# Kernel tuning notes

Measured on AMD Instinct MI355X. Metric: run time of the kernel, lower is better.

Reference implementation:

```python
import jax, jax.numpy as jnp
import numpy as np

N = 8192        # batch_size (number of nodes)
E = 262144      # number of edges
VD = 256        # vertex_dim
ED = 256        # edge_dim
HD = 512        # hid_dim
DAMPING = 0.45
EPS = 1e-5      # BatchNorm1d default eps


def setup_inputs() -> dict:
    key = jax.random.key(0)
    ks = jax.random.split(key, 8)
    def lin_w(k, out_d, in_d):
        # kaiming-uniform-ish scale, fp32
        lim = 1.0 / np.sqrt(in_d)
        return jax.random.uniform(k, (out_d, in_d), jnp.float32, -lim, lim)
    return {
        "x": jax.random.normal(ks[0], (N, VD), jnp.float32),
        "edge_weight": jax.random.normal(ks[1], (E, ED), jnp.float32),
        "edge_index": jax.random.randint(ks[2], (2, E), 0, N),
        "W0": lin_w(ks[3], HD, VD), "b0": jnp.zeros((HD,), jnp.float32),
        "Ww0": lin_w(ks[4], HD, ED), "bw0": jnp.zeros((HD,), jnp.float32),
        "W1": lin_w(ks[5], VD, HD), "b1": jnp.zeros((VD,), jnp.float32),
        "Ww1": lin_w(ks[6], ED, HD), "bw1": jnp.zeros((ED,), jnp.float32),
        "gamma": jnp.ones((HD,), jnp.float32),
        "beta": jnp.zeros((HD,), jnp.float32),
    }


def reference(x, edge_weight, edge_index, W0, b0, Ww0, bw0, W1, b1, Ww1, bw1, gamma, beta):
    out = x @ W0.T + b0                       # [N, HD]
    w = edge_weight @ Ww0.T + bw0             # [E, HD]
    src = edge_index[0]                       # [E]
    # The per-node python loop in the original is an exact segment reduction:
    # out[i] += damping * sum of w over edges with src==i (pre-update w),
    # then w[e] += damping * scalar_sum(out_new[src[e]])  (t.sum over hid dim).
    out = out + DAMPING * jax.ops.segment_sum(w, src, num_segments=N)
    node_scalar = jnp.sum(out, axis=1)        # [N] scalar per node
    w = w + DAMPING * node_scalar[src][:, None]
    # cauchy selector: cosine similarity minus identity, row-softmax mix
    nrm = jnp.sqrt(jnp.sum(out * out, axis=1, keepdims=True))   # [N,1]
    sim = (out @ out.T) / (nrm @ nrm.T) - jnp.eye(N, dtype=out.dtype)
    out = jax.nn.softmax(sim, axis=1) @ out   # [N, HD]
    # BatchNorm1d in training mode (batch stats, biased variance)
    mean = jnp.mean(w, axis=0)
    var = jnp.mean((w - mean) ** 2, axis=0)
    w = (w - mean) * jax.lax.rsqrt(var + EPS) * gamma + beta
    return out @ W1.T + b1, w @ Ww1.T + bw1
```

## Files before the change

kernel.cpp:

```cpp
#include <hip/hip_runtime.h>

typedef unsigned short u16;
typedef __attribute__((ext_vector_type(8))) short bh8;
typedef __attribute__((ext_vector_type(4))) short bh4;
typedef __attribute__((ext_vector_type(4))) float f4v;

#define NN 8192
#define EE 262144
#define VDIM 256
#define EDIM 256
#define HDIM 512
#define DAMP 0.45f

__device__ __forceinline__ float b2f(u16 u){ unsigned int x = ((unsigned int)u)<<16; return __builtin_bit_cast(float, x); }
__device__ __forceinline__ u16 f2b(float f){ unsigned int x = __builtin_bit_cast(unsigned int, f); x = (x + 0x7fffu + ((x>>16)&1u)) >> 16; return (u16)x; }

__device__ __forceinline__ void gload16(const void* g, void* l){
  __builtin_amdgcn_global_load_lds((const __attribute__((address_space(1))) void*)g,
                                   (__attribute__((address_space(3))) void*)l, 16, 0, 0);
}

__global__ __launch_bounds__(256) void k_hist(const int* __restrict__ src, int* __restrict__ deg){
  int e = blockIdx.x*256 + threadIdx.x;
  if (e < EE) atomicAdd(&deg[src[e]], 1);
}

__global__ __launch_bounds__(1024) void k_scan(const int* __restrict__ deg, int* __restrict__ ofs, int* __restrict__ cur){
  __shared__ int lds[1024];
  int t = threadIdx.x;
  int v[8], pre[8]; int s = 0;
  #pragma unroll
  for (int j=0;j<8;++j){ v[j] = deg[t*8+j]; }
  #pragma unroll
  for (int j=0;j<8;++j){ pre[j] = s; s += v[j]; }
  lds[t] = s; __syncthreads();
  int run = s;
  for (int off=1; off<1024; off<<=1){
    int x = (t>=off) ? lds[t-off] : 0;
    __syncthreads();
    lds[t] += x;
    __syncthreads();
  }
  int excl = lds[t] - run;
  #pragma unroll
  for (int j=0;j<8;++j){ int o = excl + pre[j]; ofs[t*8+j] = o; cur[t*8+j] = o; }
  if (t == 1023) ofs[NN] = excl + run;
}

__global__ __launch_bounds__(256) void k_permute(const int* __restrict__ src, int* __restrict__ cur,
                                                 int* __restrict__ pos, int* __restrict__ elist){
  int e = blockIdx.x*256 + threadIdx.x;
  if (e < EE){ int p = atomicAdd(&cur[src[e]], 1); pos[e] = p; elist[p] = e; }
}

__global__ __launch_bounds__(256) void k_cvtW(const float* __restrict__ in, u16* __restrict__ out, int n8){
  int i = blockIdx.x*256 + threadIdx.x;
  if (i < n8){
    const f4v* p = (const f4v*)(in + (size_t)i*8);
    f4v f0 = p[0], f1 = p[1];
    bh8 v;
    #pragma unroll
    for (int j=0;j<4;++j){ v[j]=(short)f2b(f0[j]); v[j+4]=(short)f2b(f1[j]); }
    ((bh8*)out)[i] = v;
  }
}

template<int A_BF16, int B_BF16, int EPI>
__global__ __launch_bounds__(256)
void k_gemm(const void* __restrict__ Aptr, const void* __restrict__ Bptr,
            int M, int N, int K, const float* __restrict__ bias,
            void* __restrict__ Cptr,
            const float* __restrict__ invnA, float* __restrict__ lsum)
{
  __shared__ u16 As[2][128*32];
  __shared__ u16 Bs[2][128*32];
  __shared__ float lrow[128];
  const int t = threadIdx.x;
  const int m0 = blockIdx.y*128, n0 = blockIdx.x*128;
  const int wid = t>>6, lane = t&63, l15 = lane&15, grp = lane>>4;
  const int wm = (wid>>1)*64, wn = (wid&1)*64;
  const int srow = t>>1, shalf = t&1;
  const int rlane = lane>>2, clane = lane&3;

  if (EPI == 3 && t < 128) lrow[t] = 0.f;

  f4v acc[4][4];
  #pragma unroll
  for (int i=0;i<4;++i)
    #pragma unroll
    for (int j=0;j<4;++j) acc[i][j] = (f4v)0.0f;

  auto stage = [&](int buf, int kt){
    if (A_BF16){
      const u16* g0 = (const u16*)Aptr + (size_t)(m0 + wid*32 + rlane)*K + kt + clane*8;
      gload16(g0,                 &As[buf][wid*1024]);
      gload16(g0 + (size_t)16*K,  &As[buf][wid*1024 + 512]);
    } else {
      u16* dst = &As[buf][srow*32 + shalf*16];
      const float* ap = (const float*)Aptr + (size_t)(m0+srow)*K + kt + shalf*16;
      const f4v* ap4 = (const f4v*)ap;
      f4v f0 = ap4[0], f1 = ap4[1], f2 = ap4[2], f3 = ap4[3];
      bh8 v0, v1;
      #pragma unroll
      for (int j=0;j<4;++j){ v0[j]=(short)f2b(f0[j]); v0[j+4]=(short)f2b(f1[j]); v1[j]=(short)f2b(f2[j]); v1[j+4]=(short)f2b(f3[j]); }
      ((bh8*)dst)[0] = v0; ((bh8*)dst)[1] = v1;
    }
    if (B_BF16){
      const u16* g0 = (const u16*)Bptr + (size_t)(n0 + wid*32 + rlane)*K + kt + clane*8;
      gload16(g0,                 &Bs[buf][wid*1024]);
      gload16(g0 + (size_t)16*K,  &Bs[buf][wid*1024 + 512]);
    } else {
      u16* dst = &Bs[buf][srow*32 + shalf*16];
      const float* bp = (const float*)Bptr + (size_t)(n0+srow)*K + kt + shalf*16;
      const f4v* bp4 = (const f4v*)bp;
      f4v f0 = bp4[0], f1 = bp4[1], f2 = bp4[2], f3 = bp4[3];
      bh8 v0, v1;
      #pragma unroll
      for (int j=0;j<4;++j){ v0[j]=(short)f2b(f0[j]); v0[j+4]=(short)f2b(f1[j]); v1[j]=(short)f2b(f2[j]); v1[j+4]=(short)f2b(f3[j]); }
      ((bh8*)dst)[0] = v0; ((bh8*)dst)[1] = v1;
    }
  };

  stage(0, 0);
  __syncthreads();
  int cur = 0;
  for (int kt=0; kt<K; kt+=32){
    if (kt + 32 < K) stage(cur^1, kt+32);
    bh8 af[4], bfv[4];
    #pragma unroll
    for (int f=0; f<4; ++f) af[f]  = *(const bh8*)&As[cur][(wm + f*16 + l15)*32 + grp*8];
    #pragma unroll
    for (int f=0; f<4; ++f) bfv[f] = *(const bh8*)&Bs[cur][(wn + f*16 + l15)*32 + grp*8];
    #pragma unroll
    for (int fi=0; fi<4; ++fi)
      #pragma unroll
      for (int fj=0; fj<4; ++fj)
        acc[fi][fj] = __builtin_amdgcn_mfma_f32_16x16x32_bf16(af[fi], bfv[fj], acc[fi][fj], 0, 0, 0);
    __syncthreads();
    cur ^= 1;
  }

  if (EPI == 3){
    float ic[4];
    #pragma unroll
    for (int fj=0; fj<4; ++fj) ic[fj] = invnA[n0 + wn + fj*16 + l15];
    #pragma unroll
    for (int fi=0; fi<4; ++fi){
      #pragma unroll
      for (int r=0;r<4;++r){
        int rowg = m0 + wm + fi*16 + grp*4 + r;
        float iq = invnA[rowg];
        float rs = 0.f;
        #pragma unroll
        for (int fj=0; fj<4; ++fj){
          int c = n0 + wn + fj*16 + l15;
          float s = acc[fi][fj][r]*iq*ic[fj];
          float p = (rowg == c) ? 1.0f : __expf(s);
          ((u16*)Cptr)[(size_t)rowg*N + c] = f2b(p);
          rs += p;
        }
        rs += __shfl_xor(rs,1); rs += __shfl_xor(rs,2); rs += __shfl_xor(rs,4); rs += __shfl_xor(rs,8);
        if (l15 == 0) atomicAdd(&lrow[wm + fi*16 + grp*4 + r], rs);
      }
    }
    __syncthreads();
    if (t < 128) lsum[(size_t)blockIdx.x*NN + m0 + t] = lrow[t];
    return;
  }

  float ilv[4][4];
  if (EPI == 4){
    #pragma unroll
    for (int fi=0; fi<4; ++fi)
      #pragma unroll
      for (int r=0;r<4;++r)
        ilv[fi][r] = 1.0f / lsum[m0 + wm + fi*16 + grp*4 + r];
  }
  #pragma unroll
  for (int fj=0; fj<4; ++fj){
    int c = n0 + wn + fj*16 + l15;
    float bv = (EPI == 0 && bias) ? bias[c] : 0.f;
    #pragma unroll
    for (int fi=0; fi<4; ++fi){
      #pragma unroll
      for (int r=0;r<4;++r){
        size_t rowg = (size_t)(m0 + wm + fi*16 + grp*4 + r);
        float v = acc[fi][fj][r];
        if (EPI == 0)      ((float*)Cptr)[rowg*N + c] = v + bv;
        else               ((u16*)Cptr)[rowg*N + c]  = f2b(v * ilv[fi][r]);
      }
    }
  }
}

__global__ __launch_bounds__(256)
void k_lred(const float* __restrict__ lpart, float* __restrict__ lsum){
  int i = blockIdx.x*256 + threadIdx.x;
  float s = 0.f;
  #pragma unroll 8
  for (int b = 0; b < 64; ++b) s += lpart[(size_t)b*NN + i];
  lsum[i] = s;
}

template<int A_BF16, int BN, int EPI>
__global__ __launch_bounds__(512, 4)
void k_gemmw3(const void* __restrict__ Aptr, const u16* __restrict__ Bptr,
              int K, const float* __restrict__ bias, void* __restrict__ Cptr,
              const int* __restrict__ mapArr, const int* __restrict__ srcIdx,
              const float* __restrict__ nsArr, const float* __restrict__ rowterm,
              const float* __restrict__ constterm)
{
  constexpr int CG = BN/64;
  constexpr int MF = (CG==8)?4:2;
  __shared__ u16 As[64*32];
  __shared__ u16 Bs[BN*32];
  const int t = threadIdx.x;
  const int tile = ((int)blockIdx.x & 7)*((int)gridDim.x>>3) + ((int)blockIdx.x>>3);
  const int m0 = tile*64;
  const int wid = t>>6, lane = t&63, l15 = lane&15, grp = lane>>4;
  const int wn = (wid & (CG-1))*64;
  const int wm = (wid / CG)*32;

  f4v acc[MF][4];
  #pragma unroll
  for (int i=0;i<MF;++i)
    #pragma unroll
    for (int j=0;j<4;++j) acc[i][j] = (f4v)0.0f;

  if (A_BF16){
    if (wid < 4){
      const u16* g0 = (const u16*)Aptr + (size_t)(m0 + wid*16 + (lane>>2))*K + (lane&3)*8;
      gload16(g0, &As[wid*512]);
    }
  } else {
    const float* ap = (const float*)Aptr + (size_t)(m0 + (t>>3))*K + (t&7)*4;
    f4v f0 = *(const f4v*)ap;
    bh4 v;
    #pragma unroll
    for (int j=0;j<4;++j) v[j]=(short)f2b(f0[j]);
    *(bh4*)&As[(t>>3)*32 + (t&7)*4] = v;
  }
  #pragma unroll
  for (int j=0;j<BN/128;++j){
    const u16* g0 = Bptr + (size_t)(j*128 + wid*16 + (lane>>2))*K + (lane&3)*8;
    gload16(g0, &Bs[wid*512 + j*4096]);
  }
  __syncthreads();

  for (int kt=0; kt<K; kt+=32){
    const bool more = (kt+32 < K);
    f4v pf; bh8 pb;
    if (more){
      if (A_BF16){
        if (t < 256)
          pb = *(const bh8*)((const u16*)Aptr + (size_t)(m0 + (t>>2))*K + kt+32 + (t&3)*8);
      } else {
        pf = *(const f4v*)((const float*)Aptr + (size_t)(m0 + (t>>3))*K + kt+32 + (t&7)*4);
      }
    }
    bh8 af[MF], bfv[4];
    #pragma unroll
    for (int f=0; f<MF; ++f) af[f]  = *(const bh8*)&As[(wm + f*16 + l15)*32 + grp*8];
    #pragma unroll
    for (int f=0; f<4; ++f)  bfv[f] = *(const bh8*)&Bs[(wn + f*16 + l15)*32 + grp*8];
    #pragma unroll
    for (int fi=0; fi<MF; ++fi)
      #pragma unroll
      for (int fj=0; fj<4; ++fj)
        acc[fi][fj] = __builtin_amdgcn_mfma_f32_16x16x32_bf16(af[fi], bfv[fj], acc[fi][fj], 0, 0, 0);
    __syncthreads();
    if (more){
      if (A_BF16){
        if (t < 256) *(bh8*)&As[(t>>2)*32 + (t&3)*8] = pb;
      } else {
        bh4 v;
        #pragma unroll
        for (int j=0;j<4;++j) v[j]=(short)f2b(pf[j]);
        *(bh4*)&As[(t>>3)*32 + (t&7)*4] = v;
      }
      #pragma unroll
      for (int j=0;j<BN/128;++j){
        const u16* g0 = Bptr + (size_t)(j*128 + wid*16 + (lane>>2))*K + kt+32 + (lane&3)*8;
        gload16(g0, &Bs[wid*512 + j*4096]);
      }
    }
    __syncthreads();
  }

  #pragma unroll
  for (int fi=0; fi<MF; ++fi){
    #pragma unroll
    for (int r=0;r<4;++r){
      int slot = m0 + wm + fi*16 + grp*4 + r;
      int mp = mapArr[slot];
      float cv = (EPI == 2) ? DAMP * nsArr[srcIdx[mp]] : 0.f;
      #pragma unroll
      for (int fj=0; fj<4; ++fj){
        int c = wn + fj*16 + l15;
        if (EPI == 5) ((u16*)Cptr)[(size_t)mp*BN + c]  = f2b(acc[fi][fj][r] + bias[c]);
        else          ((float*)Cptr)[(size_t)mp*BN + c] = acc[fi][fj][r] + cv*rowterm[c] + constterm[c];
      }
    }
  }
}

__global__ __launch_bounds__(512, 8)
void k_segsumB(const u16* __restrict__ w0, const int* __restrict__ ofs,
               float* __restrict__ S, float* __restrict__ sqpart)
{
  __shared__ u16 lds[16*512];
  const int t = threadIdx.x, w = t>>6, lane = t&63;
  const int base = blockIdx.x*128;

  int lo = 0, hi = NN-1;
  while (lo < hi){ int mid = (lo+hi+1)>>1; if (ofs[mid] <= base) lo = mid; else hi = mid-1; }
  int ni = lo;
  int nend = ofs[ni+1];

  float acc = 0.f, sqv = 0.f;
  bool first = true;

  for (int chunk = 0; chunk < 8; ++chunk){
    __syncthreads();
    {
      const u16* r0 = w0 + (size_t)(base + chunk*16 + w)*512 + lane*8;
      gload16(r0,                  &lds[w*512]);
      gload16(r0 + (size_t)8*512,  &lds[(w+8)*512]);
    }
    __syncthreads();
    #pragma unroll
    for (int r = 0; r < 16; ++r){
      int row = base + chunk*16 + r;
      float v = b2f(lds[r*512 + t]);
      acc += v; sqv += v*v;
      if (row + 1 == nend){
        if (first){ atomicAdd(&S[(size_t)ni*512 + t], acc); first = false; }
        else        S[(size_t)ni*512 + t] = acc;
        acc = 0.f; ++ni;
        while (ni < NN-1 && ofs[ni+1] == row+1) ++ni;
        nend = ofs[ni+1];
      }
    }
  }
  if (base + 128 < nend) atomicAdd(&S[(size_t)ni*512 + t], acc);
  sqpart[(size_t)blockIdx.x*512 + t] = sqv;
}

__global__ __launch_bounds__(512)
void k_sqred(const float* __restrict__ sqpart, float* __restrict__ colsumsq){
  int t = threadIdx.x;
  float s = 0.f;
  for (int b = 0; b < 32; ++b)
    s += sqpart[(size_t)(blockIdx.x*32 + b)*512 + t];
  atomicAdd(&colsumsq[t], s);
}

__global__ __launch_bounds__(256)
void k_nodefin2(const float* __restrict__ S, const float* __restrict__ out0,
                float* __restrict__ nsA, float* __restrict__ invn, u16* __restrict__ ob)
{
  const int t = threadIdx.x, wid = t>>6, lane = t&63;
  const int node = blockIdx.x*4 + wid;
  const f4v* s4 = (const f4v*)(S + (size_t)node*512 + lane*8);
  f4v sA = s4[0], sB = s4[1];
  const f4v* o4 = (const f4v*)(out0 + (size_t)node*512 + lane*8);
  f4v qA = o4[0], qB = o4[1];
  float o[8];
  #pragma unroll
  for (int j=0;j<4;++j){ o[j] = qA[j] + DAMP*sA[j]; o[j+4] = qB[j] + DAMP*sB[j]; }
  float nsp = 0.f, qp = 0.f;
  #pragma unroll
  for (int j=0;j<8;++j){ nsp += o[j]; qp += o[j]*o[j]; }
  #pragma unroll
  for (int m=1; m<64; m<<=1){ nsp += __shfl_xor(nsp, m); qp += __shfl_xor(qp, m); }
  if (lane == 0){ nsA[node] = nsp; invn[node] = rsqrtf(qp); }
  bh8 ub;
  #pragma unroll
  for (int j=0;j<8;++j) ub[j] = (short)f2b(o[j]);
  *(bh8*)(ob + (size_t)node*512 + lane*8) = ub;
}

__global__ __launch_bounds__(512)
void k_colred(const float* __restrict__ S, const float* __restrict__ nsA,
              const int* __restrict__ ofs,
              float* __restrict__ colsum0, float* __restrict__ cross,
              float* __restrict__ sumc, float* __restrict__ sumc2)
{
  __shared__ float red1[128], red2[128];
  const int t = threadIdx.x;
  const int n0 = blockIdx.x*128;
  float cs = 0.f, cr = 0.f;
  for (int i = 0; i < 128; ++i){
    int node = n0 + i;
    float s = S[(size_t)node*512 + t];
    cs += s; cr += nsA[node]*s;
  }
  atomicAdd(&colsum0[t], cs);
  atomicAdd(&cross[t],   DAMP*cr);
  if (t < 128){
    int node = n0 + t;
    float nsv = nsA[node];
    float degf = (float)(ofs[node+1] - ofs[node]);
    red1[t] = degf*nsv;
    red2[t] = degf*nsv*nsv;
  }
  __syncthreads();
  if (t == 0){
    float s1 = 0.f, s2 = 0.f;
    #pragma unroll 8
    for (int i = 0; i < 128; ++i){ s1 += red1[i]; s2 += red2[i]; }
    atomicAdd(sumc,  DAMP*s1);
    atomicAdd(sumc2, DAMP*DAMP*s2);
  }
}

__global__ __launch_bounds__(256)
void k_transpose(const u16* __restrict__ in, u16* __restrict__ out){
  __shared__ u16 tile[64][65];
  int r0 = blockIdx.x*64, c0 = blockIdx.y*64;
  int t = threadIdx.x;
  int rr = t>>2, cc = (t&3)*16;
  const u16* ip = in + (size_t)(r0+rr)*512 + c0 + cc;
  #pragma unroll
  for (int j=0;j<16;++j) tile[rr][cc+j] = ip[j];
  __syncthreads();
  int cr = t>>2, rb = (t&3)*16;
  u16* op = out + (size_t)(c0+cr)*8192 + r0 + rb;
  #pragma unroll
  for (int j=0;j<16;++j) op[j] = tile[rb+j][cr];
}

__global__ __launch_bounds__(512)
void k_bnfinal(const float* __restrict__ colsum0, const float* __restrict__ colsumsq,
               const float* __restrict__ cross, const float* __restrict__ sumc,
               const float* __restrict__ sumc2, const float* __restrict__ gamma,
               const float* __restrict__ beta, float* __restrict__ alphaA, float* __restrict__ bbA)
{
  int j = threadIdx.x;
  const float invE = 1.0f / (float)EE;
  float mean = (colsum0[j] + sumc[0]) * invE;
  float ex2  = (colsumsq[j] + 2.f*cross[j] + sumc2[0]) * invE;
  float var  = ex2 - mean*mean;
  float is   = rsqrtf(var + 1e-5f);
  float a    = gamma[j]*is;
  alphaA[j]  = a;
  bbA[j]     = beta[j] - mean*a;
}

__global__ __launch_bounds__(512)
void k_wprime(const float* __restrict__ Ww1, const float* __restrict__ alphaA,
              const float* __restrict__ bbA, const float* __restrict__ bw1,
              u16* __restrict__ Ww1pb, float* __restrict__ rowterm, float* __restrict__ constt)
{
  __shared__ float red[512];
  int k = blockIdx.x, j = threadIdx.x;
  float wv = Ww1[(size_t)k*512 + j];
  float a  = alphaA[j];
  Ww1pb[(size_t)k*512 + j] = f2b(wv*a);
  red[j] = wv*a; __syncthreads();
  for (int off=256; off>0; off>>=1){ if (j<off) red[j] += red[j+off]; __syncthreads(); }
  if (j == 0) rowterm[k] = red[0];
  __syncthreads();
  red[j] = wv*bbA[j]; __syncthreads();
  for (int off=256; off>0; off>>=1){ if (j<off) red[j] += red[j+off]; __syncthreads(); }
  if (j == 0) constt[k] = red[0] + bw1[k];
}

extern "C" void kernel_launch(void* const* d_in, const int* in_sizes, int n_in,
                              void* d_out, int out_size, void* d_ws, size_t ws_size,
                              hipStream_t stream)
{
  const float* x    = (const float*)d_in[0];
  const float* ew   = (const float*)d_in[1];
  const int*   ei   = (const int*)  d_in[2];
  const float* W0   = (const float*)d_in[3];
  const float* b0   = (const float*)d_in[4];
  const float* Ww0  = (const float*)d_in[5];
  const float* bw0  = (const float*)d_in[6];
  const float* W1   = (const float*)d_in[7];
  const float* b1   = (const float*)d_in[8];
  const float* Ww1  = (const float*)d_in[9];
  const float* bw1  = (const float*)d_in[10];
  const float* gamma= (const float*)d_in[11];
  const float* beta = (const float*)d_in[12];
  const int* src = ei;

  char* ws = (char*)d_ws;
  u16*   w0    = (u16*)  (ws + 0ULL);
  float* out0  = (float*)(ws + 268435456ULL);
  u16*   ob    = (u16*)  (ws + 285212672ULL);
  u16*   obT   = (u16*)  (ws + 293601280ULL);
  u16*   onew  = (u16*)  (ws + 301989888ULL);
  float* nsA   = (float*)(ws + 310378496ULL);
  float* invn  = (float*)(ws + 310411264ULL);
  int*   deg   = (int*)  (ws + 310444032ULL);
  int*   ofs   = (int*)  (ws + 310476800ULL);
  int*   cur   = (int*)  (ws + 310509824ULL);
  int*   elist = (int*)  (ws + 310542592ULL);
  float* stats = (float*)(ws + 311591168ULL);
  float* cross    = stats;
  float* colsum0  = stats + 512;
  float* colsumsq = stats + 1024;
  float* sumc     = stats + 1536;
  float* sumc2    = stats + 1537;
  float* lsum   = (float*)(ws + 311607552ULL);
  u16*   Ww1pb  = (u16*)  (ws + 311640320ULL);
  float* rowterm= (float*)(ws + 312164608ULL);
  float* constt = (float*)(ws + 312165632ULL);
  float* alphaA = (float*)(ws + 312166656ULL);
  float* bbA    = (float*)(ws + 312168704ULL);
  u16*   Ww0b   = (u16*)  (ws + 312170752ULL);
  int*   pos   = (int*)onew;

  float* out1 = (float*)d_out;
  float* out2 = out1 + (size_t)NN*VDIM;
  u16*   Pbuf = (u16*)out2;
  float* lpart  = (float*)((char*)out2 + 167772160ULL);
  float* sqpart = (float*)((char*)out2 + 247463936ULL);
  float* S      = (float*)((char*)out2 + 251658240ULL);

  hipMemsetAsync(deg, 0, NN*sizeof(int), stream);
  hipMemsetAsync(stats, 0, 16384, stream);
  hipMemsetAsync(S, 0, (size_t)NN*512*sizeof(float), stream);

  k_hist   <<<EE/256, 256, 0, stream>>>(src, deg);
  k_scan   <<<1, 1024, 0, stream>>>(deg, ofs, cur);
  k_permute<<<EE/256, 256, 0, stream>>>(src, cur, pos, elist);
  k_cvtW   <<<64, 256, 0, stream>>>(Ww0, Ww0b, HDIM*EDIM/8);

  k_gemmw3<0,512,5><<<4096, 512, 0, stream>>>(ew, Ww0b, EDIM, bw0, w0,
                                              pos, nullptr, nullptr, nullptr, nullptr);
  k_gemm<0,0,0><<<dim3(4,64), 256, 0, stream>>>(x, W0, NN, HDIM, VDIM, b0, out0, nullptr, nullptr);

  k_segsumB<<<2048, 512, 0, stream>>>(w0, ofs, S, sqpart);
  k_sqred  <<<64, 512, 0, stream>>>(sqpart, colsumsq);
  k_nodefin2<<<NN/4, 256, 0, stream>>>(S, out0, nsA, invn, ob);
  k_colred <<<64, 512, 0, stream>>>(S, nsA, ofs, colsum0, cross, sumc, sumc2);

  k_transpose<<<dim3(128,8), 256, 0, stream>>>(ob, obT);
  k_bnfinal<<<1, 512, 0, stream>>>(colsum0, colsumsq, cross, sumc, sumc2, gamma, beta, alphaA, bbA);
  k_wprime<<<256, 512, 0, stream>>>(Ww1, alphaA, bbA, bw1, Ww1pb, rowterm, constt);

  k_gemm<1,1,3><<<dim3(64,64), 256, 0, stream>>>(ob, ob, NN, NN, HDIM, nullptr, Pbuf, invn, lpart);
  k_lred<<<NN/256, 256, 0, stream>>>(lpart, lsum);
  k_gemm<1,1,4><<<dim3(4,64), 256, 0, stream>>>(Pbuf, obT, NN, HDIM, NN, nullptr, onew, nullptr, lsum);

  k_gemmw3<1,256,2><<<4096, 512, 0, stream>>>(w0, Ww1pb, HDIM, nullptr, out2,
                                              elist, src, nsA, rowterm, constt);
  k_gemm<1,0,0><<<dim3(2,64), 256, 0, stream>>>(onew, W1, NN, VDIM, HDIM, b1, out1, nullptr, nullptr);
}
```

Before: 805.1 us.

## Eliminate materialized edge hidden tensor via algebraic reassociation of edge linear layers

Stops materializing the E×512 edge hidden tensor w0. The segment sum is now taken over the bf16 edge inputs and then multiplied by Ww0 with a degree-scaled bias. BatchNorm sum-of-squares is computed from a 256×256 Gram matrix of the edge inputs, and the final edge GEMM uses a precomposed Ww1'·Ww0 weight with K=256 instead of 512. This removes a large GEMM and the heavy 512-wide write and reread traffic, at the cost of extra small kernels and different bf16 rounding points, which may shift accuracy.

```diff
diff --git a/kernel.cpp b/kernel.cpp
--- a/kernel.cpp
+++ b/kernel.cpp
@@ -65,12 +65,26 @@
   }
 }
 
+__global__ __launch_bounds__(256)
+void k_cvtP(const float* __restrict__ ew, const int* __restrict__ pos, u16* __restrict__ ewb){
+  int t = threadIdx.x;
+  int row = blockIdx.x*8 + (t>>5);
+  int seg = (t&31)*8;
+  const f4v* p = (const f4v*)(ew + (size_t)row*256 + seg);
+  f4v f0 = p[0], f1 = p[1];
+  bh8 v;
+  #pragma unroll
+  for (int j=0;j<4;++j){ v[j]=(short)f2b(f0[j]); v[j+4]=(short)f2b(f1[j]); }
+  *(bh8*)(ewb + (size_t)pos[row]*256 + seg) = v;
+}
+
 template<int A_BF16, int B_BF16, int EPI>
 __global__ __launch_bounds__(256)
 void k_gemm(const void* __restrict__ Aptr, const void* __restrict__ Bptr,
             int M, int N, int K, const float* __restrict__ bias,
             void* __restrict__ Cptr,
-            const float* __restrict__ invnA, float* __restrict__ lsum)
+            const float* __restrict__ invnA, float* __restrict__ lsum,
+            const int* __restrict__ ofsArg)
 {
   __shared__ u16 As[2][128*32];
   __shared__ u16 Bs[2][128*32];
@@ -176,10 +190,20 @@
       for (int r=0;r<4;++r)
         ilv[fi][r] = 1.0f / lsum[m0 + wm + fi*16 + grp*4 + r];
   }
+  float degv[4][4];
+  if (EPI == 6){
+    #pragma unroll
+    for (int fi=0; fi<4; ++fi)
+      #pragma unroll
+      for (int r=0;r<4;++r){
+        int rowg = m0 + wm + fi*16 + grp*4 + r;
+        degv[fi][r] = (float)(ofsArg[rowg+1] - ofsArg[rowg]);
+      }
+  }
   #pragma unroll
   for (int fj=0; fj<4; ++fj){
     int c = n0 + wn + fj*16 + l15;
-    float bv = (EPI == 0 && bias) ? bias[c] : 0.f;
+    float bv = ((EPI == 0 || EPI == 6) && bias) ? bias[c] : 0.f;
     #pragma unroll
     for (int fi=0; fi<4; ++fi){
       #pragma unroll
@@ -187,6 +211,7 @@
         size_t rowg = (size_t)(m0 + wm + fi*16 + grp*4 + r);
         float v = acc[fi][fj][r];
         if (EPI == 0)      ((float*)Cptr)[rowg*N + c] = v + bv;
+        else if (EPI == 6) ((float*)Cptr)[rowg*N + c] = v + degv[fi][r]*bv;
         else               ((u16*)Cptr)[rowg*N + c]  = f2b(v * ilv[fi][r]);
       }
     }
@@ -293,22 +318,21 @@
     for (int r=0;r<4;++r){
       int slot = m0 + wm + fi*16 + grp*4 + r;
       int mp = mapArr[slot];
-      float cv = (EPI == 2) ? DAMP * nsArr[srcIdx[mp]] : 0.f;
+      float cv = DAMP * nsArr[srcIdx[mp]];
       #pragma unroll
       for (int fj=0; fj<4; ++fj){
         int c = wn + fj*16 + l15;
-        if (EPI == 5) ((u16*)Cptr)[(size_t)mp*BN + c]  = f2b(acc[fi][fj][r] + bias[c]);
-        else          ((float*)Cptr)[(size_t)mp*BN + c] = acc[fi][fj][r] + cv*rowterm[c] + constterm[c];
-      }
-    }
-  }
-}
-
-__global__ __launch_bounds__(512, 8)
-void k_segsumB(const u16* __restrict__ w0, const int* __restrict__ ofs,
-               float* __restrict__ S, float* __restrict__ sqpart)
-{
-  __shared__ u16 lds[16*512];
+        ((float*)Cptr)[(size_t)mp*BN + c] = acc[fi][fj][r] + cv*rowterm[c] + constterm[c];
+      }
+    }
+  }
+}
+
+__global__ __launch_bounds__(256, 8)
+void k_segsumE(const u16* __restrict__ ewb, const int* __restrict__ ofs,
+               float* __restrict__ Sew)
+{
+  __shared__ u16 lds[16*256];
   const int t = threadIdx.x, w = t>>6, lane = t&63;
   const int base = blockIdx.x*128;
 
@@ -317,42 +341,137 @@
   int ni = lo;
   int nend = ofs[ni+1];
 
-  float acc = 0.f, sqv = 0.f;
+  float acc = 0.f;
   bool first = true;
 
   for (int chunk = 0; chunk < 8; ++chunk){
     __syncthreads();
     {
-      const u16* r0 = w0 + (size_t)(base + chunk*16 + w)*512 + lane*8;
-      gload16(r0,                  &lds[w*512]);
-      gload16(r0 + (size_t)8*512,  &lds[(w+8)*512]);
+      const u16* r0 = ewb + (size_t)(base + chunk*16 + 2*w + (lane>>5))*256 + (lane&31)*8;
+      gload16(r0,                   &lds[w*512]);
+      gload16(r0 + (size_t)8*256,   &lds[2048 + w*512]);
     }
     __syncthreads();
     #pragma unroll
     for (int r = 0; r < 16; ++r){
       int row = base + chunk*16 + r;
-      float v = b2f(lds[r*512 + t]);
-      acc += v; sqv += v*v;
+      acc += b2f(lds[r*256 + t]);
       if (row + 1 == nend){
-        if (first){ atomicAdd(&S[(size_t)ni*512 + t], acc); first = false; }
-        else        S[(size_t)ni*512 + t] = acc;
+        if (first){ atomicAdd(&Sew[(size_t)ni*256 + t], acc); first = false; }
+        else        Sew[(size_t)ni*256 + t] = acc;
         acc = 0.f; ++ni;
         while (ni < NN-1 && ofs[ni+1] == row+1) ++ni;
         nend = ofs[ni+1];
       }
     }
   }
-  if (base + 128 < nend) atomicAdd(&S[(size_t)ni*512 + t], acc);
-  sqpart[(size_t)blockIdx.x*512 + t] = sqv;
+  if (base + 128 < nend) atomicAdd(&Sew[(size_t)ni*256 + t], acc);
+}
+
+__global__ __launch_bounds__(256)
+void k_cvtS(const float* __restrict__ in, u16* __restrict__ out){
+  int i = blockIdx.x*256 + threadIdx.x;
+  const f4v* p = (const f4v*)(in + (size_t)i*8);
+  f4v f0 = p[0], f1 = p[1];
+  bh8 v;
+  #pragma unroll
+  for (int j=0;j<4;++j){ v[j]=(short)f2b(f0[j]); v[j+4]=(short)f2b(f1[j]); }
+  ((bh8*)out)[i] = v;
+}
+
+__global__ __launch_bounds__(256)
+void k_qred(const float* __restrict__ Sew, float* __restrict__ q){
+  int a = threadIdx.x;
+  float s = 0.f;
+  for (int n = blockIdx.x; n < NN; n += 32) s += Sew[(size_t)n*256 + a];
+  atomicAdd(&q[a], s);
 }
 
 __global__ __launch_bounds__(512)
-void k_sqred(const float* __restrict__ sqpart, float* __restrict__ colsumsq){
-  int t = threadIdx.x;
+void k_gram(const u16* __restrict__ ewb, float* __restrict__ Gpart)
+{
+  __shared__ u16 Xt[256*40];
+  const int t = threadIdx.x, w = t>>6, lane = t&63, l15 = lane&15, grp = lane>>4;
+  const int rowbase = (int)blockIdx.x * 1024;
+  const int sr = t>>4, cs = t&15;
+
+  f4v acc[2][16];
+  #pragma unroll
+  for (int i=0;i<2;++i)
+    #pragma unroll
+    for (int j=0;j<16;++j) acc[i][j] = (f4v)0.0f;
+
+  for (int chunk = 0; chunk < 32; ++chunk){
+    __syncthreads();
+    #pragma unroll
+    for (int i=0;i<2;++i){
+      int c0 = cs*8 + i*128;
+      bh8 v = *(const bh8*)(ewb + (size_t)(rowbase + chunk*32 + sr)*256 + c0);
+      #pragma unroll
+      for (int k=0;k<8;++k){
+        int c = c0 + k;
+        Xt[c*40 + ((sr + 8*((c>>4)&3)) & 31)] = (u16)v[k];
+      }
+    }
+    __syncthreads();
+    bh8 af[2];
+    #pragma unroll
+    for (int fa=0; fa<2; ++fa){
+      int a = w*32 + fa*16 + l15;
+      af[fa] = *(const bh8*)&Xt[a*40 + (((grp + (a>>4)) & 3) << 3)];
+    }
+    #pragma unroll
+    for (int fb=0; fb<16; ++fb){
+      int b = fb*16 + l15;
+      bh8 bf = *(const bh8*)&Xt[b*40 + (((grp + (b>>4)) & 3) << 3)];
+      #pragma unroll
+      for (int fa=0; fa<2; ++fa)
+        acc[fa][fb] = __builtin_amdgcn_mfma_f32_16x16x32_bf16(af[fa], bf, acc[fa][fb], 0, 0, 0);
+    }
+  }
+  float* Gp = Gpart + (size_t)((int)blockIdx.x & 7)*65536;
+  #pragma unroll
+  for (int fa=0; fa<2; ++fa)
+    #pragma unroll
+    for (int fb=0; fb<16; ++fb)
+      #pragma unroll
+      for (int r=0;r<4;++r)
+        atomicAdd(&Gp[(size_t)(w*32 + fa*16 + grp*4 + r)*256 + fb*16 + l15], acc[fa][fb][r]);
+}
+
+__global__ __launch_bounds__(256)
+void k_gred(const float* __restrict__ Gpart, float* __restrict__ G){
+  int i = blockIdx.x*256 + threadIdx.x;
   float s = 0.f;
-  for (int b = 0; b < 32; ++b)
-    s += sqpart[(size_t)(blockIdx.x*32 + b)*512 + t];
-  atomicAdd(&colsumsq[t], s);
+  #pragma unroll
+  for (int p=0;p<8;++p) s += Gpart[(size_t)p*65536 + i];
+  G[i] = s;
+}
+
+__global__ __launch_bounds__(256)
+void k_csq(const float* __restrict__ G, const float* __restrict__ q,
+           const float* __restrict__ Ww0, const float* __restrict__ bw0,
+           float* __restrict__ colsumsq)
+{
+  __shared__ float wj[256];
+  __shared__ float red1[256], red2[256];
+  int j = blockIdx.x, a = threadIdx.x;
+  wj[a] = Ww0[(size_t)j*256 + a];
+  __syncthreads();
+  float h = 0.f;
+  #pragma unroll 8
+  for (int b=0;b<256;++b) h += G[(size_t)a*256 + b]*wj[b];
+  red1[a] = wj[a]*h;
+  red2[a] = q[a]*wj[a];
+  __syncthreads();
+  for (int off=128; off>0; off>>=1){
+    if (a<off){ red1[a]+=red1[a+off]; red2[a]+=red2[a+off]; }
+    __syncthreads();
+  }
+  if (a==0){
+    float b0 = bw0[j];
+    colsumsq[j] = red1[0] + 2.f*b0*red2[0] + (float)EE*b0*b0;
+  }
 }
 
 __global__ __launch_bounds__(256)
@@ -450,20 +569,30 @@
 __global__ __launch_bounds__(512)
 void k_wprime(const float* __restrict__ Ww1, const float* __restrict__ alphaA,
               const float* __restrict__ bbA, const float* __restrict__ bw1,
-              u16* __restrict__ Ww1pb, float* __restrict__ rowterm, float* __restrict__ constt)
+              const float* __restrict__ bw0,
+              float* __restrict__ Ww1p, float* __restrict__ rowterm, float* __restrict__ constt)
 {
   __shared__ float red[512];
   int k = blockIdx.x, j = threadIdx.x;
   float wv = Ww1[(size_t)k*512 + j];
   float a  = alphaA[j];
-  Ww1pb[(size_t)k*512 + j] = f2b(wv*a);
+  Ww1p[(size_t)k*512 + j] = wv*a;
   red[j] = wv*a; __syncthreads();
   for (int off=256; off>0; off>>=1){ if (j<off) red[j] += red[j+off]; __syncthreads(); }
   if (j == 0) rowterm[k] = red[0];
   __syncthreads();
-  red[j] = wv*bbA[j]; __syncthreads();
+  red[j] = wv*(bbA[j] + a*bw0[j]); __syncthreads();
   for (int off=256; off>0; off>>=1){ if (j<off) red[j] += red[j+off]; __syncthreads(); }
   if (j == 0) constt[k] = red[0] + bw1[k];
+}
+
+__global__ __launch_bounds__(256)
+void k_wc(const float* __restrict__ Ww1p, const float* __restrict__ Ww0, u16* __restrict__ Wcb){
+  int k = blockIdx.x, m = threadIdx.x;
+  float s = 0.f;
+  #pragma unroll 8
+  for (int j=0;j<512;++j) s += Ww1p[(size_t)k*512+j] * Ww0[(size_t)j*256+m];
+  Wcb[(size_t)k*256+m] = f2b(s);
 }
 
 extern "C" void kernel_launch(void* const* d_in, const int* in_sizes, int n_in,
@@ -486,66 +615,80 @@
   const int* src = ei;
 
   char* ws = (char*)d_ws;
-  u16*   w0    = (u16*)  (ws + 0ULL);
-  float* out0  = (float*)(ws + 268435456ULL);
-  u16*   ob    = (u16*)  (ws + 285212672ULL);
-  u16*   obT   = (u16*)  (ws + 293601280ULL);
-  u16*   onew  = (u16*)  (ws + 301989888ULL);
-  float* nsA   = (float*)(ws + 310378496ULL);
-  float* invn  = (float*)(ws + 310411264ULL);
-  int*   deg   = (int*)  (ws + 310444032ULL);
-  int*   ofs   = (int*)  (ws + 310476800ULL);
-  int*   cur   = (int*)  (ws + 310509824ULL);
-  int*   elist = (int*)  (ws + 310542592ULL);
-  float* stats = (float*)(ws + 311591168ULL);
+  u16*   ewb   = (u16*)  (ws + 0ULL);
+  float* out0  = (float*)(ws + 134217728ULL);
+  u16*   ob    = (u16*)  (ws + 150994944ULL);
+  u16*   obT   = (u16*)  (ws + 159383552ULL);
+  u16*   onew  = (u16*)  (ws + 167772160ULL);
+  float* Sew   = (float*)(ws + 176160768ULL);
+  u16*   Sewb  = (u16*)  (ws + 184549376ULL);
+  float* S     = (float*)(ws + 188743680ULL);
+  float* Gpart = (float*)(ws + 205520896ULL);
+  float* G     = (float*)(ws + 207618048ULL);
+  float* lpart = (float*)(ws + 207880192ULL);
+  float* lsum  = (float*)(ws + 209977344ULL);
+  float* nsA   = (float*)(ws + 210010112ULL);
+  float* invn  = (float*)(ws + 210042880ULL);
+  int*   deg   = (int*)  (ws + 210075648ULL);
+  int*   ofs   = (int*)  (ws + 210108416ULL);
+  int*   cur   = (int*)  (ws + 210174208ULL);
+  int*   elist = (int*)  (ws + 210206976ULL);
+  float* stats = (float*)(ws + 211255552ULL);
   float* cross    = stats;
   float* colsum0  = stats + 512;
   float* colsumsq = stats + 1024;
   float* sumc     = stats + 1536;
   float* sumc2    = stats + 1537;
-  float* lsum   = (float*)(ws + 311607552ULL);
-  u16*   Ww1pb  = (u16*)  (ws + 311640320ULL);
-  float* rowterm= (float*)(ws + 312164608ULL);
-  float* constt = (float*)(ws + 312165632ULL);
-  float* alphaA = (float*)(ws + 312166656ULL);
-  float* bbA    = (float*)(ws + 312168704ULL);
-  u16*   Ww0b   = (u16*)  (ws + 312170752ULL);
-  int*   pos   = (int*)onew;
+  float* qvec     = stats + 2048;
+  float* Ww1p  = (float*)(ws + 211271936ULL);
+  float* rowterm=(float*)(ws + 211796224ULL);
+  float* constt =(float*)(ws + 211797248ULL);
+  float* alphaA =(float*)(ws + 211798272ULL);
+  float* bbA    =(float*)(ws + 211800320ULL);
+  u16*   Ww0b   =(u16*)  (ws + 211802368ULL);
+  u16*   Wcb    =(u16*)  (ws + 212064512ULL);
+  int*   pos    = (int*)onew;
 
   float* out1 = (float*)d_out;
   float* out2 = out1 + (size_t)NN*VDIM;
   u16*   Pbuf = (u16*)out2;
-  float* lpart  = (float*)((char*)out2 + 167772160ULL);
-  float* sqpart = (float*)((char*)out2 + 247463936ULL);
-  float* S      = (float*)((char*)out2 + 251658240ULL);
 
   hipMemsetAsync(deg, 0, NN*sizeof(int), stream);
   hipMemsetAsync(stats, 0, 16384, stream);
-  hipMemsetAsync(S, 0, (size_t)NN*512*sizeof(float), stream);
+  hipMemsetAsync(Sew, 0, (size_t)NN*256*sizeof(float), stream);
+  hipMemsetAsync(Gpart, 0, 8*65536*sizeof(float), stream);
 
   k_hist   <<<EE/256, 256, 0, stream>>>(src, deg);
   k_scan   <<<1, 1024, 0, stream>>>(deg, ofs, cur);
   k_permute<<<EE/256, 256, 0, stream>>>(src, cur, pos, elist);
   k_cvtW   <<<64, 256, 0, stream>>>(Ww0, Ww0b, HDIM*EDIM/8);
 
-  k_gemmw3<0,512,5><<<4096, 512, 0, stream>>>(ew, Ww0b, EDIM, bw0, w0,
-                                              pos, nullptr, nullptr, nullptr, nullptr);
-  k_gemm<0,0,0><<<dim3(4,64), 256, 0, stream>>>(x, W0, NN, HDIM, VDIM, b0, out0, nullptr, nullptr);
-
-  k_segsumB<<<2048, 512, 0, stream>>>(w0, ofs, S, sqpart);
-  k_sqred  <<<64, 512, 0, stream>>>(sqpart, colsumsq);
+  k_cvtP<<<EE/8, 256, 0, stream>>>(ew, pos, ewb);
+  k_gemm<0,0,0><<<dim3(4,64), 256, 0, stream>>>(x, W0, NN, HDIM, VDIM, b0, out0, nullptr, nullptr, nullptr);
+
+  k_segsumE<<<2048, 256, 0, stream>>>(ewb, ofs, Sew);
+  k_qred <<<32, 256, 0, stream>>>(Sew, qvec);
+  k_cvtS <<<NN*256/8/256, 256, 0, stream>>>(Sew, Sewb);
+  k_gemm<1,1,6><<<dim3(4,64), 256, 0, stream>>>(Sewb, Ww0b, NN, HDIM, EDIM, bw0, S, nullptr, nullptr, ofs);
+
   k_nodefin2<<<NN/4, 256, 0, stream>>>(S, out0, nsA, invn, ob);
   k_colred <<<64, 512, 0, stream>>>(S, nsA, ofs, colsum0, cross, sumc, sumc2);
 
+  k_gram<<<256, 512, 0, stream>>>(ewb, Gpart);
+  k_gred<<<256, 256, 0, stream>>>(Gpart, G);
+  k_csq <<<HDIM, 256, 0, stream>>>(G, qvec, Ww0, bw0, colsumsq);
+
+  k_bnfinal<<<1, 512, 0, stream>>>(colsum0, colsumsq, cross, sumc, sumc2, gamma, beta, alphaA, bbA);
+  k_wprime<<<256, 512, 0, stream>>>(Ww1, alphaA, bbA, bw1, bw0, Ww1p, rowterm, constt);
+  k_wc    <<<256, 256, 0, stream>>>(Ww1p, Ww0, Wcb);
+
   k_transpose<<<dim3(128,8), 256, 0, stream>>>(ob, obT);
-  k_bnfinal<<<1, 512, 0, stream>>>(colsum0, colsumsq, cross, sumc, sumc2, gamma, beta, alphaA, bbA);
-  k_wprime<<<256, 512, 0, stream>>>(Ww1, alphaA, bbA, bw1, Ww1pb, rowterm, constt);
-
-  k_gemm<1,1,3><<<dim3(64,64), 256, 0, stream>>>(ob, ob, NN, NN, HDIM, nullptr, Pbuf, invn, lpart);
+
+  k_gemm<1,1,3><<<dim3(64,64), 256, 0, stream>>>(ob, ob, NN, NN, HDIM, nullptr, Pbuf, invn, lpart, nullptr);
   k_lred<<<NN/256, 256, 0, stream>>>(lpart, lsum);
-  k_gemm<1,1,4><<<dim3(4,64), 256, 0, stream>>>(Pbuf, obT, NN, HDIM, NN, nullptr, onew, nullptr, lsum);
-
-  k_gemmw3<1,256,2><<<4096, 512, 0, stream>>>(w0, Ww1pb, HDIM, nullptr, out2,
+  k_gemm<1,1,4><<<dim3(4,64), 256, 0, stream>>>(Pbuf, obT, NN, HDIM, NN, nullptr, onew, nullptr, lsum, nullptr);
+
+  k_gemmw3<1,256,2><<<4096, 512, 0, stream>>>(ewb, Wcb, EDIM, nullptr, out2,
                                               elist, src, nsA, rowterm, constt);
-  k_gemm<1,0,0><<<dim3(2,64), 256, 0, stream>>>(onew, W1, NN, VDIM, HDIM, b1, out1, nullptr, nullptr);
-}
+  k_gemm<1,0,0><<<dim3(2,64), 256, 0, stream>>>(onew, W1, NN, VDIM, HDIM, b1, out1, nullptr, nullptr, nullptr);
+}
```

Measured after the change: 877.8 us. 1.09x slower.

## Replace P·V GEMM with dedicated 128x128 double-buffered kernel

Applied to the files above, without the earlier changes.

Swaps the generic k_gemm launch for the softmax(P)·V product (8192x512, K=8192) for a new kernel, k_pv512. It uses 512 threads, 128x128 output tiles, a 256-block grid and double-buffered LDS loaded with global_load_lds, and applies the 1/rowsum normalisation in its epilogue. The generic gemm epilogue is simplified to the fp32+bias path only. The old launch used 4x64 blocks of 256 threads over a K=8192 reduction, so the intent is better latency hiding and more data reuse. In exchange, 256 blocks may leave the CUs underfilled, and there is one barrier per 32-wide K step.

```diff
diff --git a/kernel.cpp b/kernel.cpp
--- a/kernel.cpp
+++ b/kernel.cpp
@@ -168,26 +168,16 @@
     return;
   }
 
-  float ilv[4][4];
-  if (EPI == 4){
-    #pragma unroll
-    for (int fi=0; fi<4; ++fi)
-      #pragma unroll
-      for (int r=0;r<4;++r)
-        ilv[fi][r] = 1.0f / lsum[m0 + wm + fi*16 + grp*4 + r];
-  }
   #pragma unroll
   for (int fj=0; fj<4; ++fj){
     int c = n0 + wn + fj*16 + l15;
-    float bv = (EPI == 0 && bias) ? bias[c] : 0.f;
+    float bv = (bias) ? bias[c] : 0.f;
     #pragma unroll
     for (int fi=0; fi<4; ++fi){
       #pragma unroll
       for (int r=0;r<4;++r){
         size_t rowg = (size_t)(m0 + wm + fi*16 + grp*4 + r);
-        float v = acc[fi][fj][r];
-        if (EPI == 0)      ((float*)Cptr)[rowg*N + c] = v + bv;
-        else               ((u16*)Cptr)[rowg*N + c]  = f2b(v * ilv[fi][r]);
+        ((float*)Cptr)[rowg*N + c] = acc[fi][fj][r] + bv;
       }
     }
   }
@@ -200,6 +190,67 @@
   #pragma unroll 8
   for (int b = 0; b < 64; ++b) s += lpart[(size_t)b*NN + i];
   lsum[i] = s;
+}
+
+__global__ __launch_bounds__(512, 2)
+void k_pv512(const u16* __restrict__ P, const u16* __restrict__ obT,
+             const float* __restrict__ lsum, u16* __restrict__ onew)
+{
+  __shared__ u16 As[2][128*32];
+  __shared__ u16 Bs[2][128*32];
+  const int t = threadIdx.x;
+  const int bid = (int)blockIdx.x;
+  const int tile = (bid & 7)*32 + (bid >> 3);
+  const int m0 = (tile >> 2)*128, n0 = (tile & 3)*128;
+  const int wid = t>>6, lane = t&63, l15 = lane&15, grp = lane>>4;
+  const int wm = (wid>>1)*32, wn = (wid&1)*64;
+  const int srow = t>>2, sseg = t&3;
+
+  f4v acc[2][4];
+  #pragma unroll
+  for (int i=0;i<2;++i)
+    #pragma unroll
+    for (int j=0;j<4;++j) acc[i][j] = (f4v)0.0f;
+
+  auto stage = [&](int buf, int kt){
+    const u16* gA = P   + (size_t)(m0 + srow)*NN + kt + sseg*8;
+    gload16(gA, &As[buf][wid*512]);
+    const u16* gB = obT + (size_t)(n0 + srow)*NN + kt + sseg*8;
+    gload16(gB, &Bs[buf][wid*512]);
+  };
+
+  stage(0, 0);
+  __syncthreads();
+  int cur = 0;
+  for (int kt=0; kt<NN; kt+=32){
+    if (kt + 32 < NN) stage(cur^1, kt+32);
+    bh8 af[2], bfv[4];
+    #pragma unroll
+    for (int f=0; f<2; ++f) af[f]  = *(const bh8*)&As[cur][(wm + f*16 + l15)*32 + grp*8];
+    #pragma unroll
+    for (int f=0; f<4; ++f) bfv[f] = *(const bh8*)&Bs[cur][(wn + f*16 + l15)*32 + grp*8];
+    #pragma unroll
+    for (int fi=0; fi<2; ++fi)
+      #pragma unroll
+      for (int fj=0; fj<4; ++fj)
+        acc[fi][fj] = __builtin_amdgcn_mfma_f32_16x16x32_bf16(af[fi], bfv[fj], acc[fi][fj], 0, 0, 0);
+    __syncthreads();
+    cur ^= 1;
+  }
+
+  #pragma unroll
+  for (int fi=0; fi<2; ++fi){
+    #pragma unroll
+    for (int r=0;r<4;++r){
+      int rowg = m0 + wm + fi*16 + grp*4 + r;
+      float il = 1.0f / lsum[rowg];
+      #pragma unroll
+      for (int fj=0; fj<4; ++fj){
+        int c = n0 + wn + fj*16 + l15;
+        onew[(size_t)rowg*HDIM + c] = f2b(acc[fi][fj][r] * il);
+      }
+    }
+  }
 }
 
 template<int A_BF16, int BN, int EPI>
@@ -543,7 +594,7 @@
 
   k_gemm<1,1,3><<<dim3(64,64), 256, 0, stream>>>(ob, ob, NN, NN, HDIM, nullptr, Pbuf, invn, lpart);
   k_lred<<<NN/256, 256, 0, stream>>>(lpart, lsum);
-  k_gemm<1,1,4><<<dim3(4,64), 256, 0, stream>>>(Pbuf, obT, NN, HDIM, NN, nullptr, onew, nullptr, lsum);
+  k_pv512<<<256, 512, 0, stream>>>(Pbuf, obT, lsum, onew);
 
   k_gemmw3<1,256,2><<<4096, 512, 0, stream>>>(w0, Ww1pb, HDIM, nullptr, out2,
                                               elist, src, nsA, rowterm, constt);
```

After: 756.1 us (median of 3 runs). 1.06x faster.
